# Optimization experiments

Measured on AMD Instinct MI355X. Metric: run time of the kernel, lower is better.

## Reference

```python
import jax, jax.numpy as jnp
import numpy as np

N_NODES = 50000
N_EDGES = 500000
F_IN = 128
HIDDEN = 128
N_CLASSES = 32
N_GRAPHS = 64


def setup_inputs() -> dict:
    key = jax.random.key(0)
    ks = jax.random.split(key, 16)
    x = jax.random.normal(ks[0], (N_NODES, F_IN), dtype=jnp.float32)
    edge_index = jax.random.randint(ks[1], (2, N_EDGES), 0, N_NODES, dtype=jnp.int64)
    batch = jnp.sort(jax.random.randint(ks[2], (N_NODES,), 0, N_GRAPHS, dtype=jnp.int64))
    d = {"x": x, "edge_index": edge_index, "batch": batch}
    dims = [(F_IN, HIDDEN)] + [(HIDDEN, HIDDEN)] * 4
    for i, (fi, fo) in enumerate(dims, start=1):
        s = 1.0 / np.sqrt(fi)
        d[f"W{i}"] = jax.random.uniform(ks[2 + i], (fi, fo), jnp.float32, -s, s)
        d[f"b{i}"] = jnp.zeros((fo,), jnp.float32)
    s = 1.0 / np.sqrt(HIDDEN)
    d["W_lin"] = jax.random.uniform(ks[10], (HIDDEN, N_CLASSES), jnp.float32, -s, s)
    d["b_lin"] = jnp.zeros((N_CLASSES,), jnp.float32)
    return d


def _gcn_conv(x, W, b, src, dst, norm_edge, norm_self):
    # PyG GCNConv: h = x @ W; out[dst] += norm * h[src]; + self-loop + bias
    h = x @ W
    msg = h[src] * norm_edge[:, None]                      # [E, F] gather + scale
    agg = jax.ops.segment_sum(msg, dst, num_segments=x.shape[0])  # scatter-add
    return agg + h * norm_self[:, None] + b


def reference(x, edge_index, batch, W1, b1, W2, b2, W3, b3, W4, b4, W5, b5, W_lin, b_lin):
    src, dst = edge_index[0], edge_index[1]
    n = x.shape[0]
    # degree with self-loops (in-degree at dst, +1 for the self loop)
    deg = jax.ops.segment_sum(jnp.ones_like(dst, dtype=x.dtype), dst, num_segments=n) + 1.0
    dis = jax.lax.rsqrt(deg)
    norm_edge = dis[src] * dis[dst]   # per-edge symmetric normalization
    norm_self = dis * dis             # self-loop coefficient = 1/deg

    h = jax.nn.relu(_gcn_conv(x, W1, b1, src, dst, norm_edge, norm_self))
    h = jax.nn.relu(_gcn_conv(h, W2, b2, src, dst, norm_edge, norm_self))
    h = jax.nn.relu(_gcn_conv(h, W3, b3, src, dst, norm_edge, norm_self))
    h = jax.nn.relu(_gcn_conv(h, W4, b4, src, dst, norm_edge, norm_self))
    h = _gcn_conv(h, W5, b5, src, dst, norm_edge, norm_self)

    # global mean pool over graphs in the batch
    sums = jax.ops.segment_sum(h, batch, num_segments=N_GRAPHS)
    counts = jax.ops.segment_sum(jnp.ones((n,), h.dtype), batch, num_segments=N_GRAPHS)
    pooled = sums / jnp.maximum(counts, 1.0)[:, None]
    # dropout is identity in eval mode
    return pooled @ W_lin + b_lin
```

## Files before the change

kernel.cpp:

```cpp
#include <hip/hip_runtime.h>
#include <hip/hip_bf16.h>

#define N_NODES   50000
#define N_EDGES   500000
#define FDIM      128
#define N_CLASSES 32
#define N_GRAPHS  64


__global__ void deg_kernel(const int* __restrict__ dst, int* __restrict__ deg, int E) {
    int e = blockIdx.x * blockDim.x + threadIdx.x;
    if (e < E) atomicAdd(&deg[dst[e]], 1);
}

__global__ void scan_partial(const int* __restrict__ deg, int* __restrict__ part,
                             float* __restrict__ dis, int n) {
    __shared__ int s[512];
    int t = threadIdx.x;
    int i = blockIdx.x * 512 + t;
    int d = (i < n) ? deg[i] : 0;
    if (i < n) dis[i] = rsqrtf((float)d + 1.0f);
    s[t] = d;
    __syncthreads();
    for (int o = 256; o > 0; o >>= 1) {
        if (t < o) s[t] += s[t + o];
        __syncthreads();
    }
    if (t == 0) part[blockIdx.x] = s[0];
}

__global__ void scan_offsets(int* part, int nb) {
    if (blockIdx.x == 0 && threadIdx.x == 0) {
        int acc = 0;
        for (int i = 0; i < nb; i++) { int v = part[i]; part[i] = acc; acc += v; }
    }
}

__global__ void scan_final(const int* __restrict__ deg, const int* __restrict__ part,
                           int* __restrict__ rowptr, int n) {
    __shared__ int s[512];
    int t = threadIdx.x;
    int i = blockIdx.x * 512 + t;
    int v = (i < n) ? deg[i] : 0;
    s[t] = v;
    __syncthreads();
    for (int o = 1; o < 512; o <<= 1) {
        int x = (t >= o) ? s[t - o] : 0;
        __syncthreads();
        s[t] += x;
        __syncthreads();
    }
    if (i < n) rowptr[i] = part[blockIdx.x] + s[t] - v;
}

__global__ void fill_csr(const int* __restrict__ src, const int* __restrict__ dst,
                         const int* __restrict__ rowptr, int* __restrict__ fill,
                         const float* __restrict__ dis,
                         int2* __restrict__ csr_sw, int E) {
    int e = blockIdx.x * blockDim.x + threadIdx.x;
    if (e >= E) return;
    int d = dst[e], s = src[e];
    int pos = rowptr[d] + atomicAdd(&fill[d], 1);
    float w = dis[s] * dis[d];
    csr_sw[pos] = make_int2(s, __float_as_int(w));
}


__global__ __launch_bounds__(256) void gemm32(const float* __restrict__ X,
                                              const float* __restrict__ W,
                                              float* __restrict__ H, int n) {
    __shared__ __align__(16) float xs[32][36];
    __shared__ __align__(16) float ws[32][132];
    int t = threadIdx.x;
    int ti = t & 7;
    int tj = t >> 3;
    int rowBase = blockIdx.x * 32;

    float acc[4][4];
#pragma unroll
    for (int r = 0; r < 4; r++)
#pragma unroll
        for (int c = 0; c < 4; c++) acc[r][c] = 0.f;

    for (int k0 = 0; k0 < 128; k0 += 32) {
        __syncthreads();
        {
            int r = t >> 3, kq = t & 7;
            int grow = rowBase + r;
            float4 v = make_float4(0.f, 0.f, 0.f, 0.f);
            if (grow < n) v = *(const float4*)(X + (size_t)grow * FDIM + k0 + kq * 4);
            xs[kq * 4 + 0][r] = v.x;
            xs[kq * 4 + 1][r] = v.y;
            xs[kq * 4 + 2][r] = v.z;
            xs[kq * 4 + 3][r] = v.w;
        }
        {
            int c4 = t & 31, kr = t >> 5;
#pragma unroll
            for (int p = 0; p < 4; p++) {
                int k = kr + 8 * p;
                float4 v = *(const float4*)(W + (size_t)(k0 + k) * FDIM + c4 * 4);
                *(float4*)&ws[k][c4 * 4] = v;
            }
        }
        __syncthreads();
#pragma unroll 8
        for (int k = 0; k < 32; k++) {
            float4 a = *(const float4*)&xs[k][ti * 4];
            float4 b = *(const float4*)&ws[k][tj * 4];
            float ar[4] = {a.x, a.y, a.z, a.w};
            float br[4] = {b.x, b.y, b.z, b.w};
#pragma unroll
            for (int r = 0; r < 4; r++)
#pragma unroll
                for (int c = 0; c < 4; c++) acc[r][c] = fmaf(ar[r], br[c], acc[r][c]);
        }
    }

#pragma unroll
    for (int rr = 0; rr < 4; rr++) {
        int grow = rowBase + ti * 4 + rr;
        if (grow < n) {
            float4 o = {acc[rr][0], acc[rr][1], acc[rr][2], acc[rr][3]};
            *(float4*)(H + (size_t)grow * FDIM + tj * 4) = o;
        }
    }
}


__global__ __launch_bounds__(256) void agg_kernel(const float* __restrict__ H,
                                                  float* __restrict__ OUT,
                                                  const int* __restrict__ rowptr,
                                                  const int* __restrict__ degi,
                                                  const int2* __restrict__ csr_sw,
                                                  const float* __restrict__ dis,
                                                  const float* __restrict__ bias,
                                                  int n, int relu) {
    int wid = (blockIdx.x * blockDim.x + threadIdx.x) >> 6;
    int lane = threadIdx.x & 63;
    if (wid >= n) return;
    int v = wid;
    const int2* sw = csr_sw + rowptr[v];
    int cnt = degi[v];
    float ax = 0.f, ay = 0.f;
    int e = 0;

    for (; e + 8 <= cnt; e += 8) {
        int2 p0 = sw[e + 0], p1 = sw[e + 1], p2 = sw[e + 2], p3 = sw[e + 3];
        int2 p4 = sw[e + 4], p5 = sw[e + 5], p6 = sw[e + 6], p7 = sw[e + 7];
        float2 m0 = *(const float2*)(H + (size_t)p0.x * FDIM + lane * 2);
        float2 m1 = *(const float2*)(H + (size_t)p1.x * FDIM + lane * 2);
        float2 m2 = *(const float2*)(H + (size_t)p2.x * FDIM + lane * 2);
        float2 m3 = *(const float2*)(H + (size_t)p3.x * FDIM + lane * 2);
        float2 m4 = *(const float2*)(H + (size_t)p4.x * FDIM + lane * 2);
        float2 m5 = *(const float2*)(H + (size_t)p5.x * FDIM + lane * 2);
        float2 m6 = *(const float2*)(H + (size_t)p6.x * FDIM + lane * 2);
        float2 m7 = *(const float2*)(H + (size_t)p7.x * FDIM + lane * 2);
        ax = fmaf(__int_as_float(p0.y), m0.x, ax); ay = fmaf(__int_as_float(p0.y), m0.y, ay);
        ax = fmaf(__int_as_float(p1.y), m1.x, ax); ay = fmaf(__int_as_float(p1.y), m1.y, ay);
        ax = fmaf(__int_as_float(p2.y), m2.x, ax); ay = fmaf(__int_as_float(p2.y), m2.y, ay);
        ax = fmaf(__int_as_float(p3.y), m3.x, ax); ay = fmaf(__int_as_float(p3.y), m3.y, ay);
        ax = fmaf(__int_as_float(p4.y), m4.x, ax); ay = fmaf(__int_as_float(p4.y), m4.y, ay);
        ax = fmaf(__int_as_float(p5.y), m5.x, ax); ay = fmaf(__int_as_float(p5.y), m5.y, ay);
        ax = fmaf(__int_as_float(p6.y), m6.x, ax); ay = fmaf(__int_as_float(p6.y), m6.y, ay);
        ax = fmaf(__int_as_float(p7.y), m7.x, ax); ay = fmaf(__int_as_float(p7.y), m7.y, ay);
    }
    for (; e + 4 <= cnt; e += 4) {
        int2 p0 = sw[e + 0], p1 = sw[e + 1], p2 = sw[e + 2], p3 = sw[e + 3];
        float2 m0 = *(const float2*)(H + (size_t)p0.x * FDIM + lane * 2);
        float2 m1 = *(const float2*)(H + (size_t)p1.x * FDIM + lane * 2);
        float2 m2 = *(const float2*)(H + (size_t)p2.x * FDIM + lane * 2);
        float2 m3 = *(const float2*)(H + (size_t)p3.x * FDIM + lane * 2);
        ax = fmaf(__int_as_float(p0.y), m0.x, ax); ay = fmaf(__int_as_float(p0.y), m0.y, ay);
        ax = fmaf(__int_as_float(p1.y), m1.x, ax); ay = fmaf(__int_as_float(p1.y), m1.y, ay);
        ax = fmaf(__int_as_float(p2.y), m2.x, ax); ay = fmaf(__int_as_float(p2.y), m2.y, ay);
        ax = fmaf(__int_as_float(p3.y), m3.x, ax); ay = fmaf(__int_as_float(p3.y), m3.y, ay);
    }
    for (; e < cnt; e++) {
        int2 p = sw[e];
        float2 m = *(const float2*)(H + (size_t)p.x * FDIM + lane * 2);
        ax = fmaf(__int_as_float(p.y), m.x, ax);
        ay = fmaf(__int_as_float(p.y), m.y, ay);
    }

    float dv = dis[v];
    float ns = dv * dv;
    float2 hv = *(const float2*)(H + (size_t)v * FDIM + lane * 2);
    float2 bb = *(const float2*)(bias + lane * 2);
    float ox = ax + ns * hv.x + bb.x;
    float oy = ay + ns * hv.y + bb.y;
    if (relu) { ox = fmaxf(ox, 0.f); oy = fmaxf(oy, 0.f); }
    *(float2*)(OUT + (size_t)v * FDIM + lane * 2) = make_float2(ox, oy);
}


#define POOL_BLOCKS 1024

__global__ __launch_bounds__(128) void pool_kernel(const float* __restrict__ H,
                                                   const int* __restrict__ batch,
                                                   float* __restrict__ psum,
                                                   float* __restrict__ pcnt, int n) {
    int t = threadIdx.x;
    int chunk = (n + POOL_BLOCKS - 1) / POOL_BLOCKS;
    int lo = blockIdx.x * chunk;
    int hi = lo + chunk; if (hi > n) hi = n;
    if (lo >= hi) return;

    float acc = 0.f;
    int cnt = 0;
    int curg = batch[lo];
    float hv = H[(size_t)lo * FDIM + t];
    int g = curg;
    for (int v = lo; v < hi; v++) {
        float hcur = hv;
        int gcur = g;
        if (v + 1 < hi) {
            hv = H[(size_t)(v + 1) * FDIM + t];
            g = batch[v + 1];
        }
        if (gcur != curg) {
            atomicAdd(&psum[curg * FDIM + t], acc);
            if (t == 0) atomicAdd(&pcnt[curg], (float)cnt);
            acc = 0.f; cnt = 0; curg = gcur;
        }
        acc += hcur;
        cnt++;
    }
    atomicAdd(&psum[curg * FDIM + t], acc);
    if (t == 0) atomicAdd(&pcnt[curg], (float)cnt);
}

__global__ void final_lin(const float* __restrict__ psum, const float* __restrict__ pcnt,
                          const float* __restrict__ Wl, const float* __restrict__ bl,
                          float* __restrict__ out) {
    int t = blockIdx.x * blockDim.x + threadIdx.x;
    if (t >= N_GRAPHS * N_CLASSES) return;
    int g = t >> 5, c = t & 31;
    float inv = 1.0f / fmaxf(pcnt[g], 1.0f);
    float s = 0.f;
    for (int k = 0; k < FDIM; k++) s = fmaf(psum[g * FDIM + k], Wl[k * N_CLASSES + c], s);
    out[t] = s * inv + bl[c];
}


static inline size_t align256(size_t x) { return (x + 255) & ~(size_t)255; }

extern "C" void kernel_launch(void* const* d_in, const int* in_sizes, int n_in,
                              void* d_out, int out_size, void* d_ws, size_t ws_size,
                              hipStream_t stream) {
    const float* x     = (const float*)d_in[0];
    const int*   ei    = (const int*)d_in[1];
    const int*   batch = (const int*)d_in[2];
    const float* Wls[5] = {(const float*)d_in[3], (const float*)d_in[5], (const float*)d_in[7],
                           (const float*)d_in[9], (const float*)d_in[11]};
    const float* bls[5] = {(const float*)d_in[4], (const float*)d_in[6], (const float*)d_in[8],
                           (const float*)d_in[10], (const float*)d_in[12]};
    const float* W_lin = (const float*)d_in[13];
    const float* b_lin = (const float*)d_in[14];
    float* out = (float*)d_out;

    const int N = N_NODES, E = N_EDGES;
    const int* src = ei;
    const int* dst = ei + E;

    char* p = (char*)d_ws;
    size_t off = 0;
    float* hA = (float*)(p + off); off = align256(off + (size_t)N * FDIM * 4);
    float* hB = (float*)(p + off); off = align256(off + (size_t)N * FDIM * 4);
    int2*  csr_sw = (int2*)(p + off); off = align256(off + (size_t)E * 8);
    float* dis = (float*)(p + off); off = align256(off + (size_t)N * 4);
    int*   rowptr = (int*)(p + off); off = align256(off + (size_t)N * 4);
    int*   part = (int*)(p + off); off = align256(off + 512);
    size_t zero_off = off;
    int*   deg = (int*)(p + off); off = align256(off + (size_t)N * 4);
    int*   fill = (int*)(p + off); off = align256(off + (size_t)N * 4);
    float* psum = (float*)(p + off); off = align256(off + (size_t)N_GRAPHS * FDIM * 4);
    float* pcnt = (float*)(p + off); off = align256(off + (size_t)N_GRAPHS * 4);
    size_t zero_bytes = off - zero_off;
    (void)ws_size; (void)n_in; (void)in_sizes; (void)out_size;

    hipMemsetAsync(p + zero_off, 0, zero_bytes, stream);

    deg_kernel<<<(E + 255) / 256, 256, 0, stream>>>(dst, deg, E);
    int nChunks = (N + 511) / 512;
    scan_partial<<<nChunks, 512, 0, stream>>>(deg, part, dis, N);
    scan_offsets<<<1, 64, 0, stream>>>(part, nChunks);
    scan_final<<<nChunks, 512, 0, stream>>>(deg, part, rowptr, N);
    fill_csr<<<(E + 255) / 256, 256, 0, stream>>>(src, dst, rowptr, fill, dis,
                                                  csr_sw, E);

    int gemmBlocks = (N + 31) / 32;
    int aggBlocks = (N * 64 + 255) / 256;
    const float* cur = x;
    for (int l = 0; l < 5; l++) {
        gemm32<<<gemmBlocks, 256, 0, stream>>>(cur, Wls[l], hA, N);
        int relu = (l < 4) ? 1 : 0;
        agg_kernel<<<aggBlocks, 256, 0, stream>>>(hA, hB, rowptr, deg, csr_sw,
                                                  dis, bls[l], N, relu);
        cur = hB;
    }

    pool_kernel<<<POOL_BLOCKS, 128, 0, stream>>>(hB, batch, psum, pcnt, N);
    final_lin<<<(N_GRAPHS * N_CLASSES + 255) / 256, 256, 0, stream>>>(psum, pcnt, W_lin,
                                                                      b_lin, out);
}
```

Before: 448.9 us.

## Pad CSR rows to multiples of four and enlarge GEMM row tile

Pads each node's CSR adjacency to a multiple of four edges, filled with zero-weight self entries, so the aggregation kernel drops its scalar tail loop and handles at most one 4-edge chunk after the 8-edge loop. The GEMM tile grows from 32 to 64 rows per block, with each thread computing 8x4 outputs, to improve weight reuse and cut block count. The padding adds a small extra kernel, enlarges the edge buffer, and adds extra zero-weight gathers. The larger tile raises register use.

```diff
diff --git a/kernel.cpp b/kernel.cpp
--- a/kernel.cpp
+++ b/kernel.cpp
@@ -20,7 +20,7 @@
     int i = blockIdx.x * 512 + t;
     int d = (i < n) ? deg[i] : 0;
     if (i < n) dis[i] = rsqrtf((float)d + 1.0f);
-    s[t] = d;
+    s[t] = (i < n) ? ((d + 3) & ~3) : 0;
     __syncthreads();
     for (int o = 256; o > 0; o >>= 1) {
         if (t < o) s[t] += s[t + o];
@@ -41,7 +41,7 @@
     __shared__ int s[512];
     int t = threadIdx.x;
     int i = blockIdx.x * 512 + t;
-    int v = (i < n) ? deg[i] : 0;
+    int v = (i < n) ? ((deg[i] + 3) & ~3) : 0;
     s[t] = v;
     __syncthreads();
     for (int o = 1; o < 512; o <<= 1) {
@@ -65,34 +65,47 @@
     csr_sw[pos] = make_int2(s, __float_as_int(w));
 }
 
-
-__global__ __launch_bounds__(256) void gemm32(const float* __restrict__ X,
+__global__ void pad_csr(const int* __restrict__ deg, const int* __restrict__ rowptr,
+                        int2* __restrict__ csr_sw, int n) {
+    int v = blockIdx.x * blockDim.x + threadIdx.x;
+    if (v >= n) return;
+    int d = deg[v], dp = (d + 3) & ~3;
+    int base = rowptr[v];
+    for (int i = d; i < dp; i++) csr_sw[base + i] = make_int2(v, 0);
+}
+
+
+__global__ __launch_bounds__(256) void gemm64(const float* __restrict__ X,
                                               const float* __restrict__ W,
                                               float* __restrict__ H, int n) {
-    __shared__ __align__(16) float xs[32][36];
+    __shared__ __align__(16) float xs[32][68];
     __shared__ __align__(16) float ws[32][132];
     int t = threadIdx.x;
     int ti = t & 7;
     int tj = t >> 3;
-    int rowBase = blockIdx.x * 32;
-
-    float acc[4][4];
-#pragma unroll
-    for (int r = 0; r < 4; r++)
+    int rowBase = blockIdx.x * 64;
+
+    float acc[8][4];
+#pragma unroll
+    for (int r = 0; r < 8; r++)
 #pragma unroll
         for (int c = 0; c < 4; c++) acc[r][c] = 0.f;
 
     for (int k0 = 0; k0 < 128; k0 += 32) {
         __syncthreads();
         {
-            int r = t >> 3, kq = t & 7;
-            int grow = rowBase + r;
-            float4 v = make_float4(0.f, 0.f, 0.f, 0.f);
-            if (grow < n) v = *(const float4*)(X + (size_t)grow * FDIM + k0 + kq * 4);
-            xs[kq * 4 + 0][r] = v.x;
-            xs[kq * 4 + 1][r] = v.y;
-            xs[kq * 4 + 2][r] = v.z;
-            xs[kq * 4 + 3][r] = v.w;
+            int kq = t & 7;
+#pragma unroll
+            for (int p = 0; p < 2; p++) {
+                int r = (t >> 3) + 32 * p;
+                int grow = rowBase + r;
+                float4 v = make_float4(0.f, 0.f, 0.f, 0.f);
+                if (grow < n) v = *(const float4*)(X + (size_t)grow * FDIM + k0 + kq * 4);
+                xs[kq * 4 + 0][r] = v.x;
+                xs[kq * 4 + 1][r] = v.y;
+                xs[kq * 4 + 2][r] = v.z;
+                xs[kq * 4 + 3][r] = v.w;
+            }
         }
         {
             int c4 = t & 31, kr = t >> 5;
@@ -106,20 +119,21 @@
         __syncthreads();
 #pragma unroll 8
         for (int k = 0; k < 32; k++) {
-            float4 a = *(const float4*)&xs[k][ti * 4];
+            float4 a0 = *(const float4*)&xs[k][ti * 8];
+            float4 a1 = *(const float4*)&xs[k][ti * 8 + 4];
             float4 b = *(const float4*)&ws[k][tj * 4];
-            float ar[4] = {a.x, a.y, a.z, a.w};
+            float ar[8] = {a0.x, a0.y, a0.z, a0.w, a1.x, a1.y, a1.z, a1.w};
             float br[4] = {b.x, b.y, b.z, b.w};
 #pragma unroll
-            for (int r = 0; r < 4; r++)
+            for (int r = 0; r < 8; r++)
 #pragma unroll
                 for (int c = 0; c < 4; c++) acc[r][c] = fmaf(ar[r], br[c], acc[r][c]);
         }
     }
 
 #pragma unroll
-    for (int rr = 0; rr < 4; rr++) {
-        int grow = rowBase + ti * 4 + rr;
+    for (int rr = 0; rr < 8; rr++) {
+        int grow = rowBase + ti * 8 + rr;
         if (grow < n) {
             float4 o = {acc[rr][0], acc[rr][1], acc[rr][2], acc[rr][3]};
             *(float4*)(H + (size_t)grow * FDIM + tj * 4) = o;
@@ -141,7 +155,7 @@
     if (wid >= n) return;
     int v = wid;
     const int2* sw = csr_sw + rowptr[v];
-    int cnt = degi[v];
+    int cnt = (degi[v] + 3) & ~3;
     float ax = 0.f, ay = 0.f;
     int e = 0;
 
@@ -165,7 +179,7 @@
         ax = fmaf(__int_as_float(p6.y), m6.x, ax); ay = fmaf(__int_as_float(p6.y), m6.y, ay);
         ax = fmaf(__int_as_float(p7.y), m7.x, ax); ay = fmaf(__int_as_float(p7.y), m7.y, ay);
     }
-    for (; e + 4 <= cnt; e += 4) {
+    if (e + 4 <= cnt) {
         int2 p0 = sw[e + 0], p1 = sw[e + 1], p2 = sw[e + 2], p3 = sw[e + 3];
         float2 m0 = *(const float2*)(H + (size_t)p0.x * FDIM + lane * 2);
         float2 m1 = *(const float2*)(H + (size_t)p1.x * FDIM + lane * 2);
@@ -175,12 +189,6 @@
         ax = fmaf(__int_as_float(p1.y), m1.x, ax); ay = fmaf(__int_as_float(p1.y), m1.y, ay);
         ax = fmaf(__int_as_float(p2.y), m2.x, ax); ay = fmaf(__int_as_float(p2.y), m2.y, ay);
         ax = fmaf(__int_as_float(p3.y), m3.x, ax); ay = fmaf(__int_as_float(p3.y), m3.y, ay);
-    }
-    for (; e < cnt; e++) {
-        int2 p = sw[e];
-        float2 m = *(const float2*)(H + (size_t)p.x * FDIM + lane * 2);
-        ax = fmaf(__int_as_float(p.y), m.x, ax);
-        ay = fmaf(__int_as_float(p.y), m.y, ay);
     }
 
     float dv = dis[v];
@@ -267,7 +275,7 @@
     size_t off = 0;
     float* hA = (float*)(p + off); off = align256(off + (size_t)N * FDIM * 4);
     float* hB = (float*)(p + off); off = align256(off + (size_t)N * FDIM * 4);
-    int2*  csr_sw = (int2*)(p + off); off = align256(off + (size_t)E * 8);
+    int2*  csr_sw = (int2*)(p + off); off = align256(off + ((size_t)E + 4 * N) * 8);
     float* dis = (float*)(p + off); off = align256(off + (size_t)N * 4);
     int*   rowptr = (int*)(p + off); off = align256(off + (size_t)N * 4);
     int*   part = (int*)(p + off); off = align256(off + 512);
@@ -288,12 +296,13 @@
     scan_final<<<nChunks, 512, 0, stream>>>(deg, part, rowptr, N);
     fill_csr<<<(E + 255) / 256, 256, 0, stream>>>(src, dst, rowptr, fill, dis,
                                                   csr_sw, E);
-
-    int gemmBlocks = (N + 31) / 32;
+    pad_csr<<<(N + 255) / 256, 256, 0, stream>>>(deg, rowptr, csr_sw, N);
+
+    int gemmBlocks = (N + 63) / 64;
     int aggBlocks = (N * 64 + 255) / 256;
     const float* cur = x;
     for (int l = 0; l < 5; l++) {
-        gemm32<<<gemmBlocks, 256, 0, stream>>>(cur, Wls[l], hA, N);
+        gemm64<<<gemmBlocks, 256, 0, stream>>>(cur, Wls[l], hA, N);
         int relu = (l < 4) ? 1 : 0;
         agg_kernel<<<aggBlocks, 256, 0, stream>>>(hA, hB, rowptr, deg, csr_sw,
                                                   dis, bls[l], N, relu);
```

Result: no change. 455.2 us (+1.4%).

## Pad CSR rows to multiples of four and split wavefront into half-waves with float4 gathers

Applied to the files above, without the earlier changes.

Each CSR row is padded to a multiple of four edges using zero-weight self entries, so the aggregation loop needs no scalar tail. Each wavefront is split into two 32-lane halves. Each half gathers a whole 128-float row with float4 loads and takes alternate edges, and the halves are combined with a cross-lane shuffle. The goal is wider loads and more edges in flight per iteration. The cost is extra padded entries to gather, plus a pad kernel and a larger CSR buffer.

```diff
diff --git a/kernel.cpp b/kernel.cpp
--- a/kernel.cpp
+++ b/kernel.cpp
@@ -20,7 +20,7 @@
     int i = blockIdx.x * 512 + t;
     int d = (i < n) ? deg[i] : 0;
     if (i < n) dis[i] = rsqrtf((float)d + 1.0f);
-    s[t] = d;
+    s[t] = (i < n) ? ((d + 3) & ~3) : 0;
     __syncthreads();
     for (int o = 256; o > 0; o >>= 1) {
         if (t < o) s[t] += s[t + o];
@@ -41,7 +41,7 @@
     __shared__ int s[512];
     int t = threadIdx.x;
     int i = blockIdx.x * 512 + t;
-    int v = (i < n) ? deg[i] : 0;
+    int v = (i < n) ? ((deg[i] + 3) & ~3) : 0;
     s[t] = v;
     __syncthreads();
     for (int o = 1; o < 512; o <<= 1) {
@@ -65,6 +65,15 @@
     csr_sw[pos] = make_int2(s, __float_as_int(w));
 }
 
+__global__ void pad_csr(const int* __restrict__ deg, const int* __restrict__ rowptr,
+                        int2* __restrict__ csr_sw, int n) {
+    int v = blockIdx.x * blockDim.x + threadIdx.x;
+    if (v >= n) return;
+    int d = deg[v], dp = (d + 3) & ~3;
+    int base = rowptr[v];
+    for (int i = d; i < dp; i++) csr_sw[base + i] = make_int2(v, 0);
+}
+
 
 __global__ __launch_bounds__(256) void gemm32(const float* __restrict__ X,
                                               const float* __restrict__ W,
@@ -127,6 +136,19 @@
     }
 }
 
+
+#define PGATH(I, EBASE)                                                         \
+    int2 p##I = sw[(EBASE) + 2 * (I) + half];                                   \
+    float4 m##I = *(const float4*)(H + (size_t)p##I.x * FDIM + q * 4);
+
+#define PFMA(I)                                                                 \
+    {                                                                           \
+        float w_ = __int_as_float(p##I.y);                                      \
+        acc.x = fmaf(w_, m##I.x, acc.x);                                        \
+        acc.y = fmaf(w_, m##I.y, acc.y);                                        \
+        acc.z = fmaf(w_, m##I.z, acc.z);                                        \
+        acc.w = fmaf(w_, m##I.w, acc.w);                                        \
+    }
 
 __global__ __launch_bounds__(256) void agg_kernel(const float* __restrict__ H,
                                                   float* __restrict__ OUT,
@@ -139,58 +161,51 @@
     int wid = (blockIdx.x * blockDim.x + threadIdx.x) >> 6;
     int lane = threadIdx.x & 63;
     if (wid >= n) return;
-    int v = wid;
+    int v = __builtin_amdgcn_readfirstlane(wid);
+    int half = lane >> 5;
+    int q = lane & 31;
+
     const int2* sw = csr_sw + rowptr[v];
-    int cnt = degi[v];
-    float ax = 0.f, ay = 0.f;
+    int cnt = (degi[v] + 3) & ~3;
+    float4 acc = make_float4(0.f, 0.f, 0.f, 0.f);
     int e = 0;
 
-    for (; e + 8 <= cnt; e += 8) {
-        int2 p0 = sw[e + 0], p1 = sw[e + 1], p2 = sw[e + 2], p3 = sw[e + 3];
-        int2 p4 = sw[e + 4], p5 = sw[e + 5], p6 = sw[e + 6], p7 = sw[e + 7];
-        float2 m0 = *(const float2*)(H + (size_t)p0.x * FDIM + lane * 2);
-        float2 m1 = *(const float2*)(H + (size_t)p1.x * FDIM + lane * 2);
-        float2 m2 = *(const float2*)(H + (size_t)p2.x * FDIM + lane * 2);
-        float2 m3 = *(const float2*)(H + (size_t)p3.x * FDIM + lane * 2);
-        float2 m4 = *(const float2*)(H + (size_t)p4.x * FDIM + lane * 2);
-        float2 m5 = *(const float2*)(H + (size_t)p5.x * FDIM + lane * 2);
-        float2 m6 = *(const float2*)(H + (size_t)p6.x * FDIM + lane * 2);
-        float2 m7 = *(const float2*)(H + (size_t)p7.x * FDIM + lane * 2);
-        ax = fmaf(__int_as_float(p0.y), m0.x, ax); ay = fmaf(__int_as_float(p0.y), m0.y, ay);
-        ax = fmaf(__int_as_float(p1.y), m1.x, ax); ay = fmaf(__int_as_float(p1.y), m1.y, ay);
-        ax = fmaf(__int_as_float(p2.y), m2.x, ax); ay = fmaf(__int_as_float(p2.y), m2.y, ay);
-        ax = fmaf(__int_as_float(p3.y), m3.x, ax); ay = fmaf(__int_as_float(p3.y), m3.y, ay);
-        ax = fmaf(__int_as_float(p4.y), m4.x, ax); ay = fmaf(__int_as_float(p4.y), m4.y, ay);
-        ax = fmaf(__int_as_float(p5.y), m5.x, ax); ay = fmaf(__int_as_float(p5.y), m5.y, ay);
-        ax = fmaf(__int_as_float(p6.y), m6.x, ax); ay = fmaf(__int_as_float(p6.y), m6.y, ay);
-        ax = fmaf(__int_as_float(p7.y), m7.x, ax); ay = fmaf(__int_as_float(p7.y), m7.y, ay);
-    }
-    for (; e + 4 <= cnt; e += 4) {
-        int2 p0 = sw[e + 0], p1 = sw[e + 1], p2 = sw[e + 2], p3 = sw[e + 3];
-        float2 m0 = *(const float2*)(H + (size_t)p0.x * FDIM + lane * 2);
-        float2 m1 = *(const float2*)(H + (size_t)p1.x * FDIM + lane * 2);
-        float2 m2 = *(const float2*)(H + (size_t)p2.x * FDIM + lane * 2);
-        float2 m3 = *(const float2*)(H + (size_t)p3.x * FDIM + lane * 2);
-        ax = fmaf(__int_as_float(p0.y), m0.x, ax); ay = fmaf(__int_as_float(p0.y), m0.y, ay);
-        ax = fmaf(__int_as_float(p1.y), m1.x, ax); ay = fmaf(__int_as_float(p1.y), m1.y, ay);
-        ax = fmaf(__int_as_float(p2.y), m2.x, ax); ay = fmaf(__int_as_float(p2.y), m2.y, ay);
-        ax = fmaf(__int_as_float(p3.y), m3.x, ax); ay = fmaf(__int_as_float(p3.y), m3.y, ay);
-    }
-    for (; e < cnt; e++) {
-        int2 p = sw[e];
-        float2 m = *(const float2*)(H + (size_t)p.x * FDIM + lane * 2);
-        ax = fmaf(__int_as_float(p.y), m.x, ax);
-        ay = fmaf(__int_as_float(p.y), m.y, ay);
-    }
-
-    float dv = dis[v];
-    float ns = dv * dv;
-    float2 hv = *(const float2*)(H + (size_t)v * FDIM + lane * 2);
-    float2 bb = *(const float2*)(bias + lane * 2);
-    float ox = ax + ns * hv.x + bb.x;
-    float oy = ay + ns * hv.y + bb.y;
-    if (relu) { ox = fmaxf(ox, 0.f); oy = fmaxf(oy, 0.f); }
-    *(float2*)(OUT + (size_t)v * FDIM + lane * 2) = make_float2(ox, oy);
+    for (; e + 16 <= cnt; e += 16) {
+        PGATH(0, e) PGATH(1, e) PGATH(2, e) PGATH(3, e)
+        PGATH(4, e) PGATH(5, e) PGATH(6, e) PGATH(7, e)
+        PFMA(0) PFMA(1) PFMA(2) PFMA(3) PFMA(4) PFMA(5) PFMA(6) PFMA(7)
+    }
+    if (e + 8 <= cnt) {
+        PGATH(0, e) PGATH(1, e) PGATH(2, e) PGATH(3, e)
+        PFMA(0) PFMA(1) PFMA(2) PFMA(3)
+        e += 8;
+    }
+    if (e + 4 <= cnt) {
+        PGATH(0, e) PGATH(1, e)
+        PFMA(0) PFMA(1)
+    }
+
+    acc.x += __shfl_xor(acc.x, 32);
+    acc.y += __shfl_xor(acc.y, 32);
+    acc.z += __shfl_xor(acc.z, 32);
+    acc.w += __shfl_xor(acc.w, 32);
+
+    if (half == 0) {
+        float dv = dis[v];
+        float ns = dv * dv;
+        float4 hv = *(const float4*)(H + (size_t)v * FDIM + q * 4);
+        float4 bb = *(const float4*)(bias + q * 4);
+        float4 o;
+        o.x = acc.x + ns * hv.x + bb.x;
+        o.y = acc.y + ns * hv.y + bb.y;
+        o.z = acc.z + ns * hv.z + bb.z;
+        o.w = acc.w + ns * hv.w + bb.w;
+        if (relu) {
+            o.x = fmaxf(o.x, 0.f); o.y = fmaxf(o.y, 0.f);
+            o.z = fmaxf(o.z, 0.f); o.w = fmaxf(o.w, 0.f);
+        }
+        *(float4*)(OUT + (size_t)v * FDIM + q * 4) = o;
+    }
 }
 
 
@@ -267,7 +282,7 @@
     size_t off = 0;
     float* hA = (float*)(p + off); off = align256(off + (size_t)N * FDIM * 4);
     float* hB = (float*)(p + off); off = align256(off + (size_t)N * FDIM * 4);
-    int2*  csr_sw = (int2*)(p + off); off = align256(off + (size_t)E * 8);
+    int2*  csr_sw = (int2*)(p + off); off = align256(off + ((size_t)E + 4 * N) * 8);
     float* dis = (float*)(p + off); off = align256(off + (size_t)N * 4);
     int*   rowptr = (int*)(p + off); off = align256(off + (size_t)N * 4);
     int*   part = (int*)(p + off); off = align256(off + 512);
@@ -288,6 +303,7 @@
     scan_final<<<nChunks, 512, 0, stream>>>(deg, part, rowptr, N);
     fill_csr<<<(E + 255) / 256, 256, 0, stream>>>(src, dst, rowptr, fill, dis,
                                                   csr_sw, E);
+    pad_csr<<<(N + 255) / 256, 256, 0, stream>>>(deg, rowptr, csr_sw, N);
 
     int gemmBlocks = (N + 31) / 32;
     int aggBlocks = (N * 64 + 255) / 256;
```

Measured after the change: 450.2 us. Within noise of the previous version (+0.3%).
